# Performance work log

Measured on AMD Instinct MI355X. Metric: run time of the kernel, lower is better.

The kernel has to match this reference:

```python
import jax, jax.numpy as jnp
import numpy as np

B, L, HID, H, D = 16, 512, 768, 12, 64
NUM_STRUCT = 5


def setup_inputs() -> dict:
    key = jax.random.key(0)
    ks = jax.random.split(key, 8)
    hidden_states = jax.random.normal(ks[0], (B, L, HID), jnp.float32)
    attention_mask = jnp.zeros((B, 1, 1, L), jnp.float32)  # additive mask (0 = keep)
    structure_mask = (jax.random.uniform(ks[1], (NUM_STRUCT, B, 1, L, L)) < 0.15).astype(jnp.float32)
    s = 1.0 / np.sqrt(HID).astype(np.float32)
    Wq = jax.random.normal(ks[2], (HID, HID), jnp.float32) * s
    Wk = jax.random.normal(ks[3], (HID, HID), jnp.float32) * s
    Wv = jax.random.normal(ks[4], (HID, HID), jnp.float32) * s
    bq = jnp.zeros((HID,), jnp.float32)
    bk = jnp.zeros((HID,), jnp.float32)
    bv = jnp.zeros((HID,), jnp.float32)
    # xavier-uniform-ish scale for [D,D] biaffine mats
    xav = np.sqrt(6.0 / (D + D)).astype(np.float32)
    bili = jax.random.uniform(ks[5], (NUM_STRUCT, H, D, D), jnp.float32, -xav, xav)
    abs_bias = jnp.zeros((NUM_STRUCT, H), jnp.float32)
    return {"hidden_states": hidden_states, "attention_mask": attention_mask,
            "structure_mask": structure_mask, "Wq": Wq, "bq": bq, "Wk": Wk,
            "bk": bk, "Wv": Wv, "bv": bv, "bili": bili, "abs_bias": abs_bias}


def _heads(x, b, l):
    # [B,L,HID] -> [B,H,L,D]
    return x.reshape(b, l, H, D).transpose(0, 2, 1, 3)


def reference(hidden_states, attention_mask, structure_mask, Wq, bq, Wk, bk, Wv, bv, bili, abs_bias):
    b, l, _ = hidden_states.shape
    q = _heads(hidden_states @ Wq.T + bq, b, l)  # [B,H,L,D]
    k = _heads(hidden_states @ Wk.T + bk, b, l)
    v = _heads(hidden_states @ Wv.T + bv, b, l)

    scores = jnp.einsum('bhid,bhjd->bhij', q, k)  # [B,H,L,L]
    for i in range(NUM_STRUCT):
        bias = jnp.einsum('bhip,hpq,bhjq->bhij', q, bili[i], k)
        scores = scores + (bias + abs_bias[i][None, :, None, None]) * structure_mask[i]

    scores = scores / np.sqrt(D).astype(np.float32) + attention_mask
    probs = jax.nn.softmax(scores, axis=-1)
    ctx = jnp.einsum('bhij,bhjd->bhid', probs, v)  # [B,H,L,D]
    return ctx.transpose(0, 2, 1, 3).reshape(b, l, H * D)
```

## Files before the change

kernel.cpp:

```cpp
#include <hip/hip_runtime.h>
#include <hip/hip_bf16.h>

#define BATCH 16
#define SEQ   512
#define HID   768
#define NH    12
#define HD    64
#define NS    5
#define LOG2E 1.44269504f

typedef __attribute__((ext_vector_type(8))) short short8;
typedef __attribute__((ext_vector_type(4))) short bs4;
typedef __attribute__((ext_vector_type(4))) float floatx4;

#define MFMA16(a, b, c) __builtin_amdgcn_mfma_f32_16x16x32_bf16((a), (b), (c), 0, 0, 0)

#define GLOAD16(gp, lp) __builtin_amdgcn_global_load_lds( \
    (const __attribute__((address_space(1))) unsigned*)(gp), \
    (__attribute__((address_space(3))) unsigned*)(lp), 16, 0, 0)

static __device__ __forceinline__ short f2bs(float f) {
    unsigned x = __builtin_bit_cast(unsigned, f);
    return (short)((x + 0x7fffu + ((x >> 16) & 1u)) >> 16);
}

__global__ __launch_bounds__(256) void prep_kernel(
    const float* __restrict__ hidden, const float* __restrict__ wq,
    const float* __restrict__ wk, const float* __restrict__ wv,
    const float* __restrict__ bili, const float* __restrict__ smask,
    short* __restrict__ xb, short* __restrict__ Wb, short* __restrict__ bltb,
    uchar4* __restrict__ mpk)
{
    __shared__ short Tl[64][72];
    const int bid = blockIdx.x, tid = threadIdx.x;

    if (bid < 3072) {
        int i = bid * 256 + tid;
        float4 a = ((const float4*)hidden)[2 * i];
        float4 b = ((const float4*)hidden)[2 * i + 1];
        short8 o;
        o[0] = f2bs(a.x); o[1] = f2bs(a.y); o[2] = f2bs(a.z); o[3] = f2bs(a.w);
        o[4] = f2bs(b.x); o[5] = f2bs(b.y); o[6] = f2bs(b.z); o[7] = f2bs(b.w);
        ((short8*)xb)[i] = o;
    } else if (bid < 3936) {
        int seg = bid - 3072;
        int mat = seg / 288, blk = seg % 288;
        const float* src = (mat == 0) ? wq : (mat == 1) ? wk : wv;
        int i = blk * 256 + tid;
        float4 a = ((const float4*)src)[2 * i];
        float4 b = ((const float4*)src)[2 * i + 1];
        short8 o;
        o[0] = f2bs(a.x); o[1] = f2bs(a.y); o[2] = f2bs(a.z); o[3] = f2bs(a.w);
        o[4] = f2bs(b.x); o[5] = f2bs(b.y); o[6] = f2bs(b.z); o[7] = f2bs(b.w);
        ((short8*)(Wb + (size_t)mat * HID * HID))[i] = o;
    } else if (bid < 3996) {
        int sh = bid - 3936;
        const float* src = bili + (size_t)sh * 4096;
        short* dst = bltb + (size_t)sh * 4096;
        for (int t = tid; t < 4096; t += 256) Tl[t >> 6][t & 63] = f2bs(src[t]);
        __syncthreads();
        for (int t = tid; t < 4096; t += 256) dst[t] = Tl[t & 63][t >> 6];
    } else {
        int i = (bid - 3996) * 256 + tid;
        const size_t BLL4 = (size_t)BATCH * SEQ * SEQ / 4;
        const float4* f = (const float4*)smask;
        unsigned b0 = 0, b1 = 0, b2 = 0, b3 = 0;
#pragma unroll
        for (int s = 0; s < NS; ++s) {
            float4 v = f[(size_t)s * BLL4 + i];
            b0 |= (v.x != 0.f) ? (1u << s) : 0u;
            b1 |= (v.y != 0.f) ? (1u << s) : 0u;
            b2 |= (v.z != 0.f) ? (1u << s) : 0u;
            b3 |= (v.w != 0.f) ? (1u << s) : 0u;
        }
        mpk[i] = make_uchar4((unsigned char)b0, (unsigned char)b1, (unsigned char)b2, (unsigned char)b3);
    }
}

__global__ __launch_bounds__(256) void proj_mfma(
    const short* __restrict__ xb, const short* __restrict__ Wb,
    const float* __restrict__ bq, const float* __restrict__ bk, const float* __restrict__ bv,
    short* __restrict__ qo, short* __restrict__ ko, short* __restrict__ vto)
{
    __shared__ short SMEM[16384];
    short* As = SMEM;
    short* Bs = SMEM + 4096;

    const int tid = threadIdx.x, lane = tid & 63, w = tid >> 6;
    const int q4 = lane >> 4, c15 = lane & 15;
    const int m0 = blockIdx.x * 128, n0 = blockIdx.y * 128;
    const int wrow = (w & 1) * 64, wcol = (w >> 1) * 64;

    const int srow = lane >> 2;
    const int scol = (lane & 3) * 8;
    const short* gA = xb + (size_t)(m0 + w * 32 + srow) * HID + scol;
    const short* gB = Wb + (size_t)(n0 + w * 32 + srow) * HID + scol;
    short* lA = As + w * 1024;
    short* lB = Bs + w * 1024;

    floatx4 acc[4][4];
#pragma unroll
    for (int i = 0; i < 4; ++i)
#pragma unroll
        for (int j = 0; j < 4; ++j) acc[i][j] = (floatx4){0.f, 0.f, 0.f, 0.f};

    for (int k0 = 0; k0 < HID; k0 += 32) {
        __syncthreads();
        GLOAD16(gA + k0,            lA);
        GLOAD16(gA + k0 + 16 * HID, lA + 512);
        GLOAD16(gB + k0,            lB);
        GLOAD16(gB + k0 + 16 * HID, lB + 512);
        __syncthreads();

        short8 af[4], bf[4];
#pragma unroll
        for (int ri = 0; ri < 4; ++ri)
            af[ri] = *(const short8*)&As[(wrow + ri * 16 + c15) * 32 + q4 * 8];
#pragma unroll
        for (int ci = 0; ci < 4; ++ci)
            bf[ci] = *(const short8*)&Bs[(wcol + ci * 16 + c15) * 32 + q4 * 8];
#pragma unroll
        for (int ri = 0; ri < 4; ++ri)
#pragma unroll
            for (int ci = 0; ci < 4; ++ci)
                acc[ri][ci] = MFMA16(af[ri], bf[ci], acc[ri][ci]);
    }

    __syncthreads();

    short* Sw = SMEM + w * 4096;

    const int matq = n0 / HID;
    const float* bias = (matq == 0) ? bq : (matq == 1) ? bk : bv;
    const int nmBase = (n0 - matq * HID) + wcol;
    const int h = nmBase >> 6;
    const int mg0 = m0 + wrow;
    const int bb = mg0 >> 9, l0 = mg0 & 511;

    if (matq < 2) {
        const float qsc = (matq == 0) ? (0.125f * LOG2E) : 1.0f;
#pragma unroll
        for (int ci = 0; ci < 4; ++ci) {
            const int col = ci * 16 + c15;
            const float bv2 = bias[nmBase + col];
#pragma unroll
            for (int ri = 0; ri < 4; ++ri)
#pragma unroll
                for (int r = 0; r < 4; ++r) {
                    const int row = ri * 16 + q4 * 4 + r;
                    const int phys = (row << 6) + ((((col >> 3) ^ (row & 7)) << 3) | (col & 7));
                    Sw[phys] = f2bs((acc[ri][ci][r] + bv2) * qsc);
                }
        }
        short* dst = (matq == 0) ? qo : ko;
#pragma unroll
        for (int it2 = 0; it2 < 8; ++it2) {
            const int row = it2 * 8 + (lane >> 3);
            const int g = lane & 7;
            short8 val = *(const short8*)&Sw[(row << 6) + ((g ^ (row & 7)) << 3)];
            *(short8*)&dst[(((size_t)bb * NH + h) * SEQ + (l0 + row)) * HD + g * 8] = val;
        }
    } else {
#pragma unroll
        for (int ci = 0; ci < 4; ++ci) {
            const int d = ci * 16 + c15;
            const float bv2 = bias[nmBase + d];
#pragma unroll
            for (int ri = 0; ri < 4; ++ri) {
                bs4 v4;
#pragma unroll
                for (int r = 0; r < 4; ++r) v4[r] = f2bs(acc[ri][ci][r] + bv2);
                const int lbase = ri * 16 + q4 * 4;
                const int phys = (d << 6) + ((((lbase >> 3) ^ (d & 7)) << 3) | (lbase & 7));
                *(bs4*)&Sw[phys] = v4;
            }
        }
#pragma unroll
        for (int it2 = 0; it2 < 8; ++it2) {
            const int d = it2 * 8 + (lane >> 3);
            const int g = lane & 7;
            short8 val = *(const short8*)&Sw[(d << 6) + ((g ^ (d & 7)) << 3)];
            *(short8*)&vto[(((size_t)bb * NH + h) * HD + d) * SEQ + l0 + g * 8] = val;
        }
    }
}

__global__ __launch_bounds__(256) void attn_mfma(
    const short* __restrict__ q, const short* __restrict__ k, const short* __restrict__ vt,
    const unsigned char* __restrict__ mp, const float* __restrict__ amask,
    const short* __restrict__ bilit, const float* __restrict__ abs_bias,
    float* __restrict__ out)
{
    __shared__ short Ks[64 * 72];
    __shared__ short Vs[64 * 72];
    __shared__ short Pw[4][16 * 72];
    __shared__ float abt[32];

    const int idx = blockIdx.x;
    const int bh = idx % 192, it = idx / 192;
    const int b = bh / NH, h = bh % NH;
    const int i0 = it * 64;
    const int tid = threadIdx.x, lane = tid & 63, w = tid >> 6;
    const int q4 = lane >> 4, c15 = lane & 15;

    const short* qg = q + (size_t)bh * SEQ * HD;
    const short* kg = k + (size_t)bh * SEQ * HD;
    const short* vg = vt + (size_t)bh * HD * SEQ;

    if (tid < 32) {
        float a = 0.f;
#pragma unroll
        for (int s = 0; s < NS; ++s)
            if (tid & (1u << s)) a += abs_bias[s * NH + h];
        abt[tid] = a * (0.125f * LOG2E) - 23.0f;
    }
    __syncthreads();

    short8 aQ0 = *(const short8*)&qg[(size_t)(i0 + w * 16 + c15) * HD + q4 * 8];
    short8 aQ1 = *(const short8*)&qg[(size_t)(i0 + w * 16 + c15) * HD + 32 + q4 * 8];

    short* pw = &Pw[w][0];
    short8 aP[NS][2];
#pragma unroll
    for (int s = 0; s < NS; ++s) {
        const short* bt = bilit + ((size_t)s * NH + h) * 4096;
#pragma unroll
        for (int ns = 0; ns < 4; ++ns) {
            short8 bf0 = *(const short8*)&bt[(ns * 16 + c15) * 64 + q4 * 8];
            short8 bf1 = *(const short8*)&bt[(ns * 16 + c15) * 64 + 32 + q4 * 8];
            floatx4 acc = {0.f, 0.f, 0.f, 0.f};
            acc = MFMA16(aQ0, bf0, acc);
            acc = MFMA16(aQ1, bf1, acc);
#pragma unroll
            for (int r = 0; r < 4; ++r)
                pw[(q4 * 4 + r) * 72 + ns * 16 + c15] = f2bs(acc[r]);
        }
        aP[s][0] = *(const short8*)&pw[c15 * 72 + q4 * 8];
        aP[s][1] = *(const short8*)&pw[c15 * 72 + 32 + q4 * 8];
    }

    float l_part[4] = {0.f, 0.f, 0.f, 0.f};
    floatx4 O[4];
#pragma unroll
    for (int d = 0; d < 4; ++d) O[d] = (floatx4){0.f, 0.f, 0.f, 0.f};

    const int ibase = i0 + w * 16 + q4 * 4;
    const unsigned char* mbp = mp + (size_t)b * SEQ * SEQ + (size_t)ibase * SEQ + c15;
    const float* amrow = amask + b * SEQ;

    for (int jt = 0; jt < 8; ++jt) {
        const int j0 = jt * 64;
        __syncthreads();
        for (int c = tid; c < 512; c += 256) {
            int r = c >> 3, o = (c & 7) * 8;
            *(short8*)&Ks[r * 72 + o] = *(const short8*)&kg[(size_t)(j0 + r) * HD + o];
            *(short8*)&Vs[r * 72 + o] = *(const short8*)&vg[(size_t)r * SEQ + j0 + o];
        }
        __syncthreads();

#pragma unroll
        for (int js = 0; js < 4; ++js) {
            const int jr = j0 + js * 16;
            short8 kf0 = *(const short8*)&Ks[(js * 16 + c15) * 72 + q4 * 8];
            short8 kf1 = *(const short8*)&Ks[(js * 16 + c15) * 72 + 32 + q4 * 8];

            floatx4 a0 = {0.f, 0.f, 0.f, 0.f};
            a0 = MFMA16(aQ0, kf0, a0);
            a0 = MFMA16(aQ1, kf1, a0);
            floatx4 as_[NS];
#pragma unroll
            for (int s = 0; s < NS; ++s) {
                floatx4 t = {0.f, 0.f, 0.f, 0.f};
                t = MFMA16(aP[s][0], kf0, t);
                t = MFMA16(aP[s][1], kf1, t);
                as_[s] = t;
            }
            const float am = amrow[jr + c15] * LOG2E;
#pragma unroll
            for (int r = 0; r < 4; ++r) {
                unsigned mb = mbp[r * SEQ + jr];
                float sc = a0[r] + am + abt[mb & 31];
#pragma unroll
                for (int s = 0; s < NS; ++s)
                    sc = fmaf((float)((mb >> s) & 1u), as_[s][r], sc);
                float p = __builtin_amdgcn_exp2f(sc);
                l_part[r] += p;
                pw[(q4 * 4 + r) * 72 + (js & 1) * 16 + c15] = f2bs(p);
            }
            if (js & 1) {
                short8 pA = *(const short8*)&pw[c15 * 72 + q4 * 8];
                const int kk = js >> 1;
#pragma unroll
                for (int d = 0; d < 4; ++d) {
                    short8 vb = *(const short8*)&Vs[(d * 16 + c15) * 72 + kk * 32 + q4 * 8];
                    O[d] = MFMA16(pA, vb, O[d]);
                }
            }
        }
    }

#pragma unroll
    for (int r = 0; r < 4; ++r) {
        float l = l_part[r];
        l += __shfl_xor(l, 1);
        l += __shfl_xor(l, 2);
        l += __shfl_xor(l, 4);
        l += __shfl_xor(l, 8);
        float inv = 1.f / l;
        float* orow = out + ((size_t)b * SEQ + ibase + r) * HID + h * HD;
#pragma unroll
        for (int d = 0; d < 4; ++d)
            orow[d * 16 + c15] = O[d][r] * inv;
    }
}

extern "C" void kernel_launch(void* const* d_in, const int* in_sizes, int n_in,
                              void* d_out, int out_size, void* d_ws, size_t ws_size,
                              hipStream_t stream) {
    const float* hidden   = (const float*)d_in[0];
    const float* amask    = (const float*)d_in[1];
    const float* smask    = (const float*)d_in[2];
    const float* Wq       = (const float*)d_in[3];
    const float* bq       = (const float*)d_in[4];
    const float* Wk       = (const float*)d_in[5];
    const float* bk       = (const float*)d_in[6];
    const float* Wv       = (const float*)d_in[7];
    const float* bv       = (const float*)d_in[8];
    const float* bili     = (const float*)d_in[9];
    const float* abs_bias = (const float*)d_in[10];
    float* out = (float*)d_out;

    char* ws = (char*)d_ws;
    const size_t QKV = (size_t)BATCH * NH * SEQ * HD * 2;
    short* qb   = (short*)(ws);
    short* kb   = (short*)(ws + QKV);
    short* vtb  = (short*)(ws + 2 * QKV);
    short* xb   = (short*)(ws + 3 * QKV);
    short* Wb   = (short*)(ws + 4 * QKV);
    short* bltb = (short*)(ws + 4 * QKV + (size_t)3 * HID * HID * 2);
    unsigned char* mpk = (unsigned char*)(ws + 4 * QKV + (size_t)3 * HID * HID * 2
                                          + (size_t)NS * NH * HD * HD * 2);

    prep_kernel<<<8092, 256, 0, stream>>>(hidden, Wq, Wk, Wv, bili, smask,
                                          xb, Wb, bltb, (uchar4*)mpk);

    proj_mfma<<<dim3(BATCH * SEQ / 128, 3 * HID / 128), 256, 0, stream>>>(
        xb, Wb, bq, bk, bv, qb, kb, vtb);

    attn_mfma<<<(SEQ / 64) * NH * BATCH, 256, 0, stream>>>(
        qb, kb, vtb, mpk, amask, bltb, abs_bias, out);
}
```

Baseline: 333.2 us.

## Transpose packed mask and double-buffer K/V via async LDS loads in attention

The mask-packing stage now writes the 5-bit structure mask transposed (j-major), staged through shared memory, so each lane in the attention kernel fetches four row bytes with a single 32-bit load, prefetched one tile ahead. K and V tiles are double-buffered through global_load_lds with an XOR swizzle in place of the padded synchronous copies, letting the next tile's load overlap the current tile's MFMA work. The additive mask is cached in LDS, the P scratch buffer shrinks, and launch bounds request 4 blocks per SM. The risks are a synchronisation hazard in the async-load double buffer (only one barrier per iteration, with no visible wait on the async loads) and register pressure from the occupancy hint.

```diff
diff --git a/kernel.cpp b/kernel.cpp
--- a/kernel.cpp
+++ b/kernel.cpp
@@ -29,7 +29,7 @@
     const float* __restrict__ wk, const float* __restrict__ wv,
     const float* __restrict__ bili, const float* __restrict__ smask,
     short* __restrict__ xb, short* __restrict__ Wb, short* __restrict__ bltb,
-    uchar4* __restrict__ mpk)
+    unsigned char* __restrict__ mT)
 {
     __shared__ short Tl[64][72];
     const int bid = blockIdx.x, tid = threadIdx.x;
@@ -61,19 +61,35 @@
         __syncthreads();
         for (int t = tid; t < 4096; t += 256) dst[t] = Tl[t & 63][t >> 6];
     } else {
-        int i = (bid - 3996) * 256 + tid;
-        const size_t BLL4 = (size_t)BATCH * SEQ * SEQ / 4;
-        const float4* f = (const float4*)smask;
-        unsigned b0 = 0, b1 = 0, b2 = 0, b3 = 0;
+        int t = bid - 3996;
+        int b = t >> 6;
+        int tile = t & 63;
+        int ib0 = (tile >> 3) * 64, jb0 = (tile & 7) * 64;
+        unsigned char* Tb = (unsigned char*)Tl;
+        const int ii = tid >> 2, jj0 = (tid & 3) * 16;
+        const size_t BLL = (size_t)BATCH * SEQ * SEQ;
+        const float* sm = smask + (size_t)b * SEQ * SEQ + (size_t)(ib0 + ii) * SEQ + jb0 + jj0;
+        unsigned char bytes[16];
+#pragma unroll
+        for (int jj = 0; jj < 16; ++jj) bytes[jj] = 0;
 #pragma unroll
         for (int s = 0; s < NS; ++s) {
-            float4 v = f[(size_t)s * BLL4 + i];
-            b0 |= (v.x != 0.f) ? (1u << s) : 0u;
-            b1 |= (v.y != 0.f) ? (1u << s) : 0u;
-            b2 |= (v.z != 0.f) ? (1u << s) : 0u;
-            b3 |= (v.w != 0.f) ? (1u << s) : 0u;
-        }
-        mpk[i] = make_uchar4((unsigned char)b0, (unsigned char)b1, (unsigned char)b2, (unsigned char)b3);
+            const float4* f = (const float4*)(sm + (size_t)s * BLL);
+#pragma unroll
+            for (int g = 0; g < 4; ++g) {
+                float4 v = f[g];
+                bytes[g * 4 + 0] |= (unsigned char)((v.x != 0.f) ? (1u << s) : 0u);
+                bytes[g * 4 + 1] |= (unsigned char)((v.y != 0.f) ? (1u << s) : 0u);
+                bytes[g * 4 + 2] |= (unsigned char)((v.z != 0.f) ? (1u << s) : 0u);
+                bytes[g * 4 + 3] |= (unsigned char)((v.w != 0.f) ? (1u << s) : 0u);
+            }
+        }
+#pragma unroll
+        for (int jj = 0; jj < 16; ++jj) Tb[(jj0 + jj) * 80 + ii] = bytes[jj];
+        __syncthreads();
+        const int jT = tid >> 2, iseg = (tid & 3) * 16;
+        uint4 val = *(const uint4*)&Tb[jT * 80 + iseg];
+        *(uint4*)&mT[((size_t)b * SEQ + jb0 + jT) * SEQ + ib0 + iseg] = val;
     }
 }
 
@@ -185,15 +201,16 @@
     }
 }
 
-__global__ __launch_bounds__(256) void attn_mfma(
+__global__ __launch_bounds__(256, 4) void attn_mfma(
     const short* __restrict__ q, const short* __restrict__ k, const short* __restrict__ vt,
-    const unsigned char* __restrict__ mp, const float* __restrict__ amask,
+    const unsigned char* __restrict__ mT, const float* __restrict__ amask,
     const short* __restrict__ bilit, const float* __restrict__ abs_bias,
     float* __restrict__ out)
 {
-    __shared__ short Ks[64 * 72];
-    __shared__ short Vs[64 * 72];
-    __shared__ short Pw[4][16 * 72];
+    __shared__ short KsB[2][4096];
+    __shared__ short VsB[2][4096];
+    __shared__ short Pw[4][16 * 40];
+    __shared__ float Am[SEQ];
     __shared__ float abt[32];
 
     const int idx = blockIdx.x;
@@ -201,12 +218,22 @@
     const int b = bh / NH, h = bh % NH;
     const int i0 = it * 64;
     const int tid = threadIdx.x, lane = tid & 63, w = tid >> 6;
-    const int q4 = lane >> 4, c15 = lane & 15;
+    const int q4 = lane >> 4, c15 = lane & 15, x7 = c15 & 7;
 
     const short* qg = q + (size_t)bh * SEQ * HD;
     const short* kg = k + (size_t)bh * SEQ * HD;
     const short* vg = vt + (size_t)bh * HD * SEQ;
 
+    const int s0 = w * 128 + lane;
+    const int r0 = s0 >> 3, cg0 = (s0 & 7) ^ (r0 & 7);
+    const int s1 = s0 + 64;
+    const int r1 = s1 >> 3, cg1 = (s1 & 7) ^ (r1 & 7);
+
+    GLOAD16(kg + (size_t)r0 * HD + cg0 * 8, &KsB[0][w * 1024]);
+    GLOAD16(kg + (size_t)r1 * HD + cg1 * 8, &KsB[0][w * 1024 + 512]);
+    GLOAD16(vg + (size_t)r0 * SEQ + cg0 * 8, &VsB[0][w * 1024]);
+    GLOAD16(vg + (size_t)r1 * SEQ + cg1 * 8, &VsB[0][w * 1024 + 512]);
+
     if (tid < 32) {
         float a = 0.f;
 #pragma unroll
@@ -214,7 +241,7 @@
             if (tid & (1u << s)) a += abs_bias[s * NH + h];
         abt[tid] = a * (0.125f * LOG2E) - 23.0f;
     }
-    __syncthreads();
+    for (int c = tid; c < SEQ; c += 256) Am[c] = amask[b * SEQ + c] * LOG2E;
 
     short8 aQ0 = *(const short8*)&qg[(size_t)(i0 + w * 16 + c15) * HD + q4 * 8];
     short8 aQ1 = *(const short8*)&qg[(size_t)(i0 + w * 16 + c15) * HD + 32 + q4 * 8];
@@ -225,18 +252,21 @@
     for (int s = 0; s < NS; ++s) {
         const short* bt = bilit + ((size_t)s * NH + h) * 4096;
 #pragma unroll
-        for (int ns = 0; ns < 4; ++ns) {
-            short8 bf0 = *(const short8*)&bt[(ns * 16 + c15) * 64 + q4 * 8];
-            short8 bf1 = *(const short8*)&bt[(ns * 16 + c15) * 64 + 32 + q4 * 8];
-            floatx4 acc = {0.f, 0.f, 0.f, 0.f};
-            acc = MFMA16(aQ0, bf0, acc);
-            acc = MFMA16(aQ1, bf1, acc);
-#pragma unroll
-            for (int r = 0; r < 4; ++r)
-                pw[(q4 * 4 + r) * 72 + ns * 16 + c15] = f2bs(acc[r]);
-        }
-        aP[s][0] = *(const short8*)&pw[c15 * 72 + q4 * 8];
-        aP[s][1] = *(const short8*)&pw[c15 * 72 + 32 + q4 * 8];
+        for (int half = 0; half < 2; ++half) {
+#pragma unroll
+            for (int n2 = 0; n2 < 2; ++n2) {
+                const int ns = half * 2 + n2;
+                short8 bf0 = *(const short8*)&bt[(ns * 16 + c15) * 64 + q4 * 8];
+                short8 bf1 = *(const short8*)&bt[(ns * 16 + c15) * 64 + 32 + q4 * 8];
+                floatx4 acc = {0.f, 0.f, 0.f, 0.f};
+                acc = MFMA16(aQ0, bf0, acc);
+                acc = MFMA16(aQ1, bf1, acc);
+#pragma unroll
+                for (int r = 0; r < 4; ++r)
+                    pw[(q4 * 4 + r) * 40 + n2 * 16 + c15] = f2bs(acc[r]);
+            }
+            aP[s][half] = *(const short8*)&pw[c15 * 40 + q4 * 8];
+        }
     }
 
     float l_part[4] = {0.f, 0.f, 0.f, 0.f};
@@ -245,24 +275,39 @@
     for (int d = 0; d < 4; ++d) O[d] = (floatx4){0.f, 0.f, 0.f, 0.f};
 
     const int ibase = i0 + w * 16 + q4 * 4;
-    const unsigned char* mbp = mp + (size_t)b * SEQ * SEQ + (size_t)ibase * SEQ + c15;
-    const float* amrow = amask + b * SEQ;
+    const unsigned char* mTb = mT + (size_t)b * SEQ * SEQ;
+
+    unsigned mv[4];
+#pragma unroll
+    for (int js = 0; js < 4; ++js)
+        mv[js] = *(const unsigned*)&mTb[(size_t)(js * 16 + c15) * SEQ + ibase];
 
     for (int jt = 0; jt < 8; ++jt) {
         const int j0 = jt * 64;
         __syncthreads();
-        for (int c = tid; c < 512; c += 256) {
-            int r = c >> 3, o = (c & 7) * 8;
-            *(short8*)&Ks[r * 72 + o] = *(const short8*)&kg[(size_t)(j0 + r) * HD + o];
-            *(short8*)&Vs[r * 72 + o] = *(const short8*)&vg[(size_t)r * SEQ + j0 + o];
-        }
-        __syncthreads();
+
+        unsigned mvn[4];
+        if (jt < 7) {
+            const int jn = j0 + 64;
+            short* kb_ = &KsB[(jt + 1) & 1][w * 1024];
+            short* vb_ = &VsB[(jt + 1) & 1][w * 1024];
+            GLOAD16(kg + (size_t)(jn + r0) * HD + cg0 * 8, kb_);
+            GLOAD16(kg + (size_t)(jn + r1) * HD + cg1 * 8, kb_ + 512);
+            GLOAD16(vg + (size_t)r0 * SEQ + jn + cg0 * 8, vb_);
+            GLOAD16(vg + (size_t)r1 * SEQ + jn + cg1 * 8, vb_ + 512);
+#pragma unroll
+            for (int js = 0; js < 4; ++js)
+                mvn[js] = *(const unsigned*)&mTb[(size_t)(jn + js * 16 + c15) * SEQ + ibase];
+        }
+
+        const short* Kc = KsB[jt & 1];
+        const short* Vc = VsB[jt & 1];
 
 #pragma unroll
         for (int js = 0; js < 4; ++js) {
-            const int jr = j0 + js * 16;
-            short8 kf0 = *(const short8*)&Ks[(js * 16 + c15) * 72 + q4 * 8];
-            short8 kf1 = *(const short8*)&Ks[(js * 16 + c15) * 72 + 32 + q4 * 8];
+            const int row = js * 16 + c15;
+            short8 kf0 = *(const short8*)&Kc[row * 64 + ((q4 ^ x7) << 3)];
+            short8 kf1 = *(const short8*)&Kc[row * 64 + (((4 + q4) ^ x7) << 3)];
 
             floatx4 a0 = {0.f, 0.f, 0.f, 0.f};
             a0 = MFMA16(aQ0, kf0, a0);
@@ -270,33 +315,36 @@
             floatx4 as_[NS];
 #pragma unroll
             for (int s = 0; s < NS; ++s) {
-                floatx4 t = {0.f, 0.f, 0.f, 0.f};
-                t = MFMA16(aP[s][0], kf0, t);
-                t = MFMA16(aP[s][1], kf1, t);
-                as_[s] = t;
-            }
-            const float am = amrow[jr + c15] * LOG2E;
+                floatx4 tacc = {0.f, 0.f, 0.f, 0.f};
+                tacc = MFMA16(aP[s][0], kf0, tacc);
+                tacc = MFMA16(aP[s][1], kf1, tacc);
+                as_[s] = tacc;
+            }
+            const float amv = Am[j0 + js * 16 + c15];
 #pragma unroll
             for (int r = 0; r < 4; ++r) {
-                unsigned mb = mbp[r * SEQ + jr];
-                float sc = a0[r] + am + abt[mb & 31];
+                const unsigned mbyte = (mv[js] >> (8 * r)) & 0xffu;
+                float sc = a0[r] + amv + abt[mbyte & 31u];
 #pragma unroll
                 for (int s = 0; s < NS; ++s)
-                    sc = fmaf((float)((mb >> s) & 1u), as_[s][r], sc);
+                    sc = fmaf((float)((mbyte >> s) & 1u), as_[s][r], sc);
                 float p = __builtin_amdgcn_exp2f(sc);
                 l_part[r] += p;
-                pw[(q4 * 4 + r) * 72 + (js & 1) * 16 + c15] = f2bs(p);
+                pw[(q4 * 4 + r) * 40 + (js & 1) * 16 + c15] = f2bs(p);
             }
             if (js & 1) {
-                short8 pA = *(const short8*)&pw[c15 * 72 + q4 * 8];
+                short8 pA = *(const short8*)&pw[c15 * 40 + q4 * 8];
                 const int kk = js >> 1;
 #pragma unroll
                 for (int d = 0; d < 4; ++d) {
-                    short8 vb = *(const short8*)&Vs[(d * 16 + c15) * 72 + kk * 32 + q4 * 8];
+                    const int vrow = d * 16 + c15;
+                    short8 vb = *(const short8*)&Vc[vrow * 64 + (((kk * 4 + q4) ^ x7) << 3)];
                     O[d] = MFMA16(pA, vb, O[d]);
                 }
             }
         }
+#pragma unroll
+        for (int js = 0; js < 4; ++js) mv[js] = mvn[js];
     }
 
 #pragma unroll
@@ -338,15 +386,15 @@
     short* xb   = (short*)(ws + 3 * QKV);
     short* Wb   = (short*)(ws + 4 * QKV);
     short* bltb = (short*)(ws + 4 * QKV + (size_t)3 * HID * HID * 2);
-    unsigned char* mpk = (unsigned char*)(ws + 4 * QKV + (size_t)3 * HID * HID * 2
-                                          + (size_t)NS * NH * HD * HD * 2);
-
-    prep_kernel<<<8092, 256, 0, stream>>>(hidden, Wq, Wk, Wv, bili, smask,
-                                          xb, Wb, bltb, (uchar4*)mpk);
+    unsigned char* mT = (unsigned char*)(ws + 4 * QKV + (size_t)3 * HID * HID * 2
+                                         + (size_t)NS * NH * HD * HD * 2);
+
+    prep_kernel<<<5020, 256, 0, stream>>>(hidden, Wq, Wk, Wv, bili, smask,
+                                          xb, Wb, bltb, mT);
 
     proj_mfma<<<dim3(BATCH * SEQ / 128, 3 * HID / 128), 256, 0, stream>>>(
         xb, Wb, bq, bk, bv, qb, kb, vtb);
 
     attn_mfma<<<(SEQ / 64) * NH * BATCH, 256, 0, stream>>>(
-        qb, kb, vtb, mpk, amask, bltb, abs_bias, out);
+        qb, kb, vtb, mT, amask, bltb, abs_bias, out);
 }
```

New measurement: 388.3 us. 1.17x slower.
